# Kernel optimization log

Measured on AMD Instinct MI355X. Metric: run time of the kernel, lower is better.

## Reference

```python
import jax, jax.numpy as jnp
import numpy as np

HK, WK = 7, 11  # local_k


def _local_mask(H, W):
    # Equivalent to the torch buffer: 0 inside the hk x wk window centered on the
    # query position (for odd hk, wk), -inf outside. Shape (N, N), N = H*W.
    n = jnp.arange(H * W)
    hq, wq = n // W, n % W
    dh = jnp.abs(hq[:, None] - hq[None, :])
    dw = jnp.abs(wq[:, None] - wq[None, :])
    allowed = (dh <= HK // 2) & (dw <= WK // 2)
    return jnp.where(allowed, 0.0, -jnp.inf).astype(jnp.float32)


def setup_inputs() -> dict:
    key = jax.random.key(0)
    k1, k2, k3 = jax.random.split(key, 3)
    B, H, W, C = 8, 32, 64, 512
    N = H * W
    x = jax.random.normal(k1, (B, N, C), dtype=jnp.float32)
    qkv_w = jax.random.normal(k2, (3 * C, C), dtype=jnp.float32) * (C ** -0.5)
    proj_w = jax.random.normal(k3, (C, C), dtype=jnp.float32) * (C ** -0.5)
    proj_b = jnp.zeros((C,), dtype=jnp.float32)
    return {"x": x, "qkv_w": qkv_w, "proj_w": proj_w, "proj_b": proj_b, "H": H, "W": W}


def reference(x, qkv_w, proj_w, proj_b, H, W):
    B, N, C = x.shape
    num_heads = 8
    head_dim = C // num_heads
    scale = head_dim ** -0.5

    # qkv: Linear(dim, 3*dim, bias=False) -> (B, N, 3, heads, head_dim)
    qkv = (x @ qkv_w.T).reshape(B, N, 3, num_heads, head_dim)
    q = qkv[:, :, 0].transpose(0, 2, 1, 3) * scale  # (B, h, N, d)
    k = qkv[:, :, 1].transpose(0, 2, 1, 3)
    v = qkv[:, :, 2].transpose(0, 2, 1, 3)

    attn = jnp.einsum('bhnd,bhmd->bhnm', q, k)  # (B, h, N, N)
    attn = attn + _local_mask(H, W)  # broadcast over (B, h)
    attn = jax.nn.softmax(attn, axis=-1)

    out = jnp.einsum('bhnm,bhmd->bhnd', attn, v)  # (B, h, N, d)
    out = out.transpose(0, 2, 1, 3).reshape(B, N, C)
    return out @ proj_w.T + proj_b
```

## Files before the change

kernel.cpp:

```cpp
#include <hip/hip_runtime.h>
#include <hip/hip_bf16.h>

#define B_SZ 8
#define H_SZ 32
#define W_SZ 64
#define N_SZ 2048
#define C_SZ 512
#define NH 8
#define HD 64

using u16 = unsigned short;
typedef __attribute__((ext_vector_type(8))) short s16x8;
typedef __attribute__((ext_vector_type(4))) float f32x4;

__device__ __forceinline__ float bf2f(u16 u) {
    union { unsigned int i; float f; } c; c.i = ((unsigned int)u) << 16; return c.f;
}
__device__ __forceinline__ u16 f2bf(float f) {
    union { float f; unsigned int i; } c; c.f = f;
    unsigned int r = c.i + 0x7fffu + ((c.i >> 16) & 1u);
    return (u16)(r >> 16);
}

#define GLL16(gp, lp) __builtin_amdgcn_global_load_lds( \
    (const __attribute__((address_space(1))) unsigned int*)(gp), \
    (__attribute__((address_space(3))) unsigned int*)(lp), 16, 0, 0)

__device__ __forceinline__ int lds_off(int row, int chunk) {
    return (row * 8 + (chunk ^ (row & 7))) * 8;
}

#define NX4 2097152
#define NQ4 196608
#define NP4 65536
__global__ __launch_bounds__(256)
void conv_all(const float* __restrict__ x, const float* __restrict__ qw,
              const float* __restrict__ pw, u16* __restrict__ xb,
              u16* __restrict__ qwb, u16* __restrict__ pwb)
{
    const int i = blockIdx.x * 256 + threadIdx.x;
    const float* src; u16* dst; int idx; float sc = 1.0f;
    if (i < NX4)             { src = x;  dst = xb;  idx = i; }
    else if (i < NX4 + NQ4)  { src = qw; dst = qwb; idx = i - NX4;
                               if (idx < 65536) sc = 0.125f; }
    else                     { src = pw; dst = pwb; idx = i - NX4 - NQ4; }
    const float4 v = ((const float4*)src)[idx];
    ushort4 o = { f2bf(v.x * sc), f2bf(v.y * sc), f2bf(v.z * sc), f2bf(v.w * sc) };
    ((ushort4*)dst)[idx] = o;
}

template<int MODE, int NT>
__global__ __launch_bounds__(256)
void gemm_mfma(const u16* __restrict__ A, const u16* __restrict__ Bw,
               const float* __restrict__ bias,
               u16* __restrict__ q_ws, u16* __restrict__ k_ws, u16* __restrict__ v_ws,
               float* __restrict__ outp, int K)
{
    constexpr int NJ = (NT == 128) ? 4 : 2;
    __shared__ u16 As[128 * 64];
    __shared__ u16 Bs[NT * 64];
    const int t    = threadIdx.x;
    const int m0   = blockIdx.x * 128;
    const int n0   = blockIdx.y * NT;
    const int wave = t >> 6, lane = t & 63;
    const int wm   = (wave >> 1) << 6;
    const int wn   = (wave & 1) * (NJ * 16);
    const int l16  = lane & 15, quad = lane >> 4;
    const int srow = t >> 3;
    const int sch  = (t & 7) ^ (srow & 7);

    constexpr int AD0 = (MODE == 0) ? 4 : 2;
    f32x4 acc[AD0][4] = {};

    for (int k0 = 0; k0 < K; k0 += 64) {
        __syncthreads();
        #pragma unroll
        for (int g = 0; g < 4; ++g)
            GLL16(A + (size_t)(m0 + 32 * g + srow) * K + k0 + sch * 8,
                  &As[g * 2048 + t * 8]);
        #pragma unroll
        for (int g = 0; g < NT / 32; ++g)
            GLL16(Bw + (size_t)(n0 + 32 * g + srow) * K + k0 + sch * 8,
                  &Bs[g * 2048 + t * 8]);
        __syncthreads();

        s16x8 fx[4][2], fw[NJ][2];
        #pragma unroll
        for (int i = 0; i < 4; ++i) {
            const int R = wm + 16 * i + l16;
            fx[i][0] = *(const s16x8*)&As[lds_off(R, quad)];
            fx[i][1] = *(const s16x8*)&As[lds_off(R, 4 + quad)];
        }
        #pragma unroll
        for (int j = 0; j < NJ; ++j) {
            const int R = wn + 16 * j + l16;
            fw[j][0] = *(const s16x8*)&Bs[lds_off(R, quad)];
            fw[j][1] = *(const s16x8*)&Bs[lds_off(R, 4 + quad)];
        }
        if (MODE == 1 || n0 < 1024) {
            #pragma unroll
            for (int w = 0; w < AD0; ++w)
                #pragma unroll
                for (int x = 0; x < 4; ++x) {
                    acc[w][x] = __builtin_amdgcn_mfma_f32_16x16x32_bf16(fw[w][0], fx[x][0], acc[w][x], 0, 0, 0);
                    acc[w][x] = __builtin_amdgcn_mfma_f32_16x16x32_bf16(fw[w][1], fx[x][1], acc[w][x], 0, 0, 0);
                }
        } else {
            #pragma unroll
            for (int x = 0; x < 4; ++x)
                #pragma unroll
                for (int w = 0; w < 4; ++w) {
                    acc[x][w] = __builtin_amdgcn_mfma_f32_16x16x32_bf16(fx[x][0], fw[w][0], acc[x][w], 0, 0, 0);
                    acc[x][w] = __builtin_amdgcn_mfma_f32_16x16x32_bf16(fx[x][1], fw[w][1], acc[x][w], 0, 0, 0);
                }
        }
    }

    if (MODE == 0) {
        const int bb = m0 >> 11;
        if (n0 < 1024) {
            const int h = ((n0 + wn) >> 6) & 7;
            u16* T  = (n0 < 512) ? q_ws : k_ws;
            u16* tb = T + ((size_t)bb * NH + h) * (N_SZ * HD);
            const int nn0 = (m0 & 2047) + wm;
            const int dd0 = (quad << 2);
            #pragma unroll
            for (int w = 0; w < 4; ++w)
                #pragma unroll
                for (int x = 0; x < 4; ++x) {
                    const int nn = nn0 + 16 * x + l16;
                    ushort4 st = { f2bf(acc[w][x][0]), f2bf(acc[w][x][1]),
                                   f2bf(acc[w][x][2]), f2bf(acc[w][x][3]) };
                    *(ushort4*)(tb + (size_t)nn * HD + 16 * w + dd0) = st;
                }
        } else {
            const int nnb = (m0 & 2047) + wm + (quad << 2);
            #pragma unroll
            for (int w = 0; w < 4; ++w) {
                const int c = n0 - 1024 + wn + 16 * w + l16;
                const int h = c >> 6, dd = c & 63;
                u16* vp = v_ws + (((size_t)bb * NH + h) * HD + dd) * N_SZ + nnb;
                #pragma unroll
                for (int x = 0; x < 4; ++x) {
                    ushort4 st = { f2bf(acc[x][w][0]), f2bf(acc[x][w][1]),
                                   f2bf(acc[x][w][2]), f2bf(acc[x][w][3]) };
                    *(ushort4*)(vp + 16 * x) = st;
                }
            }
        }
    } else {
        #pragma unroll
        for (int w = 0; w < 2; ++w) {
            const int cb = n0 + wn + 16 * w + (quad << 2);
            const float4 bv = *(const float4*)&bias[cb];
            #pragma unroll
            for (int x = 0; x < 4; ++x) {
                const int gm = m0 + wm + 16 * x + l16;
                float4 st = { acc[w][x][0] + bv.x, acc[w][x][1] + bv.y,
                              acc[w][x][2] + bv.z, acc[w][x][3] + bv.w };
                *(float4*)&outp[(size_t)gm * C_SZ + cb] = st;
            }
        }
    }
}

__global__ __launch_bounds__(256)
void attn_mfma(const u16* __restrict__ q_ws, const u16* __restrict__ k_ws,
               const u16* __restrict__ vt_ws, u16* __restrict__ o_ws)
{
    __shared__ u16 KV[2][64 * 64];
    __shared__ u16 Ps[4][16 * 40];

    const int t = threadIdx.x, wave = t >> 6, lane = t & 63;
    const int l16 = lane & 15, quad = lane >> 4;
    const int u  = blockIdx.x;
    const int p  = u & 15;
    const int bh = u >> 4;
    const int r0 = 2 * p, r1 = 2 * p + 1;
    const size_t base = (size_t)bh * (N_SZ * HD);
    const int srow = t >> 3;
    const int sch  = (t & 7) ^ (srow & 7);

    const u16* qg = q_ws + base + (size_t)r0 * (64 * HD);
    u16* Qst = &KV[0][0];
    #pragma unroll
    for (int g = 0; g < 4; ++g)
        GLL16(qg + (size_t)(srow + 32 * g) * 64 + sch * 8, Qst + g * 2048 + t * 8);
    __syncthreads();

    s16x8 aQ[2][2];
    #pragma unroll
    for (int s = 0; s < 2; ++s) {
        const int Rq = 64 * s + 16 * wave + l16;
        aQ[s][0] = *(const s16x8*)&Qst[lds_off(Rq, quad)];
        aQ[s][1] = *(const s16x8*)&Qst[lds_off(Rq, 4 + quad)];
    }

    const int kb = min(max(16 * wave - 8, 0), 32);

    f32x4 accO[2][4] = {};
    float lp[2][4] = {};

    const int hlo = (r0 - 3 < 0) ? 0 : r0 - 3;
    const int hhi = (r1 + 3 > H_SZ - 1) ? H_SZ - 1 : r1 + 3;

    for (int hh = hlo; hh <= hhi; ++hh) {
        __syncthreads();
        const u16* kg = k_ws + base + (size_t)hh * (64 * HD);
        GLL16(kg + (size_t)srow        * 64 + sch * 8, &KV[0][t * 8]);
        GLL16(kg + (size_t)(srow + 32) * 64 + sch * 8, &KV[0][2048 + t * 8]);
        const u16* vg = vt_ws + base + (size_t)hh * 64;
        GLL16(vg + (size_t)srow        * N_SZ + sch * 8, &KV[1][t * 8]);
        GLL16(vg + (size_t)(srow + 32) * N_SZ + sch * 8, &KV[1][2048 + t * 8]);
        __syncthreads();

        s16x8 bK[2][2];
        #pragma unroll
        for (int j = 0; j < 2; ++j) {
            const int Rk = kb + 16 * j + l16;
            bK[j][0] = *(const s16x8*)&KV[0][lds_off(Rk, quad)];
            bK[j][1] = *(const s16x8*)&KV[0][lds_off(Rk, 4 + quad)];
        }
        s16x8 vf[4];
        #pragma unroll
        for (int j = 0; j < 4; ++j)
            vf[j] = *(const s16x8*)&KV[1][lds_off(16 * j + l16, (kb >> 3) + quad)];

        #pragma unroll
        for (int s = 0; s < 2; ++s) {
            const int dh = hh - (r0 + s);
            if (dh * dh > 9) continue;
            f32x4 z[2] = {{0.f,0.f,0.f,0.f},{0.f,0.f,0.f,0.f}};
            #pragma unroll
            for (int j = 0; j < 2; ++j) {
                z[j] = __builtin_amdgcn_mfma_f32_16x16x32_bf16(aQ[s][0], bK[j][0], z[j], 0, 0, 0);
                z[j] = __builtin_amdgcn_mfma_f32_16x16x32_bf16(aQ[s][1], bK[j][1], z[j], 0, 0, 0);
            }
            #pragma unroll
            for (int j = 0; j < 2; ++j) {
                const int ww = kb + 16 * j + l16;
                #pragma unroll
                for (int r = 0; r < 4; ++r) {
                    const int dw = ww - (16 * wave + quad * 4 + r);
                    const float pv = (dw * dw <= 25) ? __expf(z[j][r]) : 0.f;
                    const u16 pb = f2bf(pv);
                    lp[s][r] += bf2f(pb);
                    Ps[wave][(quad * 4 + r) * 40 + 16 * j + l16] = pb;
                }
            }
            s16x8 aP = *(const s16x8*)&Ps[wave][l16 * 40 + quad * 8];
            #pragma unroll
            for (int j = 0; j < 4; ++j)
                accO[s][j] = __builtin_amdgcn_mfma_f32_16x16x32_bf16(vf[j], aP, accO[s][j], 0, 0, 0);
        }
    }

    #pragma unroll
    for (int s = 0; s < 2; ++s)
        #pragma unroll
        for (int r = 0; r < 4; ++r) {
            lp[s][r] += __shfl_xor(lp[s][r], 1);
            lp[s][r] += __shfl_xor(lp[s][r], 2);
            lp[s][r] += __shfl_xor(lp[s][r], 4);
            lp[s][r] += __shfl_xor(lp[s][r], 8);
        }

    const int srcl = (l16 >> 2) << 4;
    const int rr   = l16 & 3;
    float inv[2];
    #pragma unroll
    for (int s = 0; s < 2; ++s) {
        const float a0 = __shfl(lp[s][0], srcl);
        const float a1 = __shfl(lp[s][1], srcl);
        const float a2 = __shfl(lp[s][2], srcl);
        const float a3 = __shfl(lp[s][3], srcl);
        const float lq = (rr == 0) ? a0 : (rr == 1) ? a1 : (rr == 2) ? a2 : a3;
        inv[s] = 1.0f / lq;
    }

    const int bb = bh >> 3, h = bh & 7;
    #pragma unroll
    for (int s = 0; s < 2; ++s) {
        const int row = (r0 + s) * 64 + 16 * wave + l16;
        u16* ob = o_ws + ((size_t)bb * N_SZ + row) * C_SZ + h * 64 + (quad << 2);
        #pragma unroll
        for (int j = 0; j < 4; ++j) {
            ushort4 st = { f2bf(accO[s][j][0] * inv[s]), f2bf(accO[s][j][1] * inv[s]),
                           f2bf(accO[s][j][2] * inv[s]), f2bf(accO[s][j][3] * inv[s]) };
            *(ushort4*)(ob + 16 * j) = st;
        }
    }
}

extern "C" void kernel_launch(void* const* d_in, const int* in_sizes, int n_in,
                              void* d_out, int out_size, void* d_ws, size_t ws_size,
                              hipStream_t stream)
{
    const float* x      = (const float*)d_in[0];
    const float* qkv_w  = (const float*)d_in[1];
    const float* proj_w = (const float*)d_in[2];
    const float* proj_b = (const float*)d_in[3];
    float* outp = (float*)d_out;

    const size_t seg = (size_t)B_SZ * NH * N_SZ * HD;
    u16* q_ws = (u16*)d_ws;
    u16* k_ws = q_ws + seg;
    u16* v_ws = k_ws + seg;
    u16* o_ws = v_ws + seg;
    u16* xb   = o_ws + seg;
    u16* qwb  = xb + (size_t)16384 * 512;
    u16* pwb  = qwb + (size_t)1536 * 512;

    conv_all<<<9216, 256, 0, stream>>>(x, qkv_w, proj_w, xb, qwb, pwb);

    gemm_mfma<0, 128><<<dim3(128, 12), 256, 0, stream>>>(xb, qwb, nullptr,
                                                         q_ws, k_ws, v_ws, nullptr, C_SZ);
    attn_mfma<<<B_SZ * NH * (H_SZ / 2), 256, 0, stream>>>(q_ws, k_ws, v_ws, o_ws);
    gemm_mfma<1, 64><<<dim3(128, 8), 256, 0, stream>>>(o_ws, pwb, proj_b,
                                                       nullptr, nullptr, nullptr, outp, C_SZ);
}
```

Baseline: 187.8 us.

## Split GEMM into larger-tile double-buffered QKV and projection kernels

Replaces the shared templated GEMM with two specialised kernels that use 256x256 (QKV, 512 threads) and 256x128 (projection) tiles. Each loads K in 32-wide slices through a double-buffered LDS pipeline that prefetches the next slice while computing the current one. The aim is more operand reuse per tile and hidden global-load latency. In exchange the grid is much smaller (384 and 256 blocks), which may underfill the GPU's many CUs. The V output now uses scalar 16-bit transposed stores.

```diff
diff --git a/kernel.cpp b/kernel.cpp
--- a/kernel.cpp
+++ b/kernel.cpp
@@ -21,6 +21,10 @@
     unsigned int r = c.i + 0x7fffu + ((c.i >> 16) & 1u);
     return (u16)(r >> 16);
 }
+__device__ __forceinline__ ushort4 pack4(f32x4 a) {
+    ushort4 s = { f2bf(a[0]), f2bf(a[1]), f2bf(a[2]), f2bf(a[3]) };
+    return s;
+}
 
 #define GLL16(gp, lp) __builtin_amdgcn_global_load_lds( \
     (const __attribute__((address_space(1))) unsigned int*)(gp), \
@@ -28,6 +32,9 @@
 
 __device__ __forceinline__ int lds_off(int row, int chunk) {
     return (row * 8 + (chunk ^ (row & 7))) * 8;
+}
+__device__ __forceinline__ int lds_off32(int row, int chunk) {
+    return row * 32 + (chunk ^ ((row >> 1) & 3)) * 8;
 }
 
 #define NX4 2097152
@@ -49,117 +56,145 @@
     ((ushort4*)dst)[idx] = o;
 }
 
-template<int MODE, int NT>
-__global__ __launch_bounds__(256)
-void gemm_mfma(const u16* __restrict__ A, const u16* __restrict__ Bw,
-               const float* __restrict__ bias,
-               u16* __restrict__ q_ws, u16* __restrict__ k_ws, u16* __restrict__ v_ws,
-               float* __restrict__ outp, int K)
-{
-    constexpr int NJ = (NT == 128) ? 4 : 2;
-    __shared__ u16 As[128 * 64];
-    __shared__ u16 Bs[NT * 64];
-    const int t    = threadIdx.x;
-    const int m0   = blockIdx.x * 128;
-    const int n0   = blockIdx.y * NT;
-    const int wave = t >> 6, lane = t & 63;
-    const int wm   = (wave >> 1) << 6;
-    const int wn   = (wave & 1) * (NJ * 16);
-    const int l16  = lane & 15, quad = lane >> 4;
-    const int srow = t >> 3;
-    const int sch  = (t & 7) ^ (srow & 7);
-
-    constexpr int AD0 = (MODE == 0) ? 4 : 2;
-    f32x4 acc[AD0][4] = {};
-
-    for (int k0 = 0; k0 < K; k0 += 64) {
+__global__ __launch_bounds__(512, 2)
+void gemm_qkv(const u16* __restrict__ A, const u16* __restrict__ Bw,
+              u16* __restrict__ q_ws, u16* __restrict__ k_ws, u16* __restrict__ v_ws)
+{
+    __shared__ u16 As[2][256 * 32];
+    __shared__ u16 Bs[2][256 * 32];
+    const int t = threadIdx.x;
+    const int m0 = blockIdx.x * 256;
+    const int n0 = blockIdx.y * 256;
+    const int wave = t >> 6, lane = t & 63, l16 = lane & 15, quad = lane >> 4;
+    const int wm2 = wave >> 2, wn2 = wave & 3;
+    const int srow = t >> 2;
+    const int sch  = (t & 3) ^ ((srow >> 1) & 3);
+
+    f32x4 acc[4][8] = {};
+
+    GLL16(A  + (size_t)(m0 +       srow) * C_SZ + sch * 8, &As[0][t * 8]);
+    GLL16(A  + (size_t)(m0 + 128 + srow) * C_SZ + sch * 8, &As[0][4096 + t * 8]);
+    GLL16(Bw + (size_t)(n0 +       srow) * C_SZ + sch * 8, &Bs[0][t * 8]);
+    GLL16(Bw + (size_t)(n0 + 128 + srow) * C_SZ + sch * 8, &Bs[0][4096 + t * 8]);
+
+    for (int it = 0; it < 16; ++it) {
         __syncthreads();
-        #pragma unroll
-        for (int g = 0; g < 4; ++g)
-            GLL16(A + (size_t)(m0 + 32 * g + srow) * K + k0 + sch * 8,
-                  &As[g * 2048 + t * 8]);
-        #pragma unroll
-        for (int g = 0; g < NT / 32; ++g)
-            GLL16(Bw + (size_t)(n0 + 32 * g + srow) * K + k0 + sch * 8,
-                  &Bs[g * 2048 + t * 8]);
+        if (it < 15) {
+            const int kn = (it + 1) * 32;
+            u16* an = As[(it + 1) & 1]; u16* bn = Bs[(it + 1) & 1];
+            GLL16(A  + (size_t)(m0 +       srow) * C_SZ + kn + sch * 8, an + t * 8);
+            GLL16(A  + (size_t)(m0 + 128 + srow) * C_SZ + kn + sch * 8, an + 4096 + t * 8);
+            GLL16(Bw + (size_t)(n0 +       srow) * C_SZ + kn + sch * 8, bn + t * 8);
+            GLL16(Bw + (size_t)(n0 + 128 + srow) * C_SZ + kn + sch * 8, bn + 4096 + t * 8);
+        }
+        const u16* ac = As[it & 1];
+        const u16* bc = Bs[it & 1];
+        s16x8 fw[4], fx[8];
+        #pragma unroll
+        for (int j = 0; j < 4; ++j)
+            fw[j] = *(const s16x8*)&bc[lds_off32(wn2 * 64 + 16 * j + l16, quad)];
+        #pragma unroll
+        for (int i = 0; i < 8; ++i)
+            fx[i] = *(const s16x8*)&ac[lds_off32(wm2 * 128 + 16 * i + l16, quad)];
+        #pragma unroll
+        for (int j = 0; j < 4; ++j)
+            #pragma unroll
+            for (int i = 0; i < 8; ++i)
+                acc[j][i] = __builtin_amdgcn_mfma_f32_16x16x32_bf16(fw[j], fx[i], acc[j][i], 0, 0, 0);
+    }
+
+    const int bb  = m0 >> 11;
+    const int nn0 = (m0 & 2047) + wm2 * 128;
+    if (n0 < 1024) {
+        u16* T = (n0 < 512) ? q_ws : k_ws;
+        const int h = ((n0 + wn2 * 64) >> 6) & 7;
+        u16* tb = T + ((size_t)bb * NH + h) * (N_SZ * HD);
+        #pragma unroll
+        for (int j = 0; j < 4; ++j) {
+            const int dd = 16 * j + (quad << 2);
+            #pragma unroll
+            for (int i = 0; i < 8; ++i) {
+                const int nn = nn0 + 16 * i + l16;
+                *(ushort4*)(tb + (size_t)nn * HD + dd) = pack4(acc[j][i]);
+            }
+        }
+    } else {
+        const int h = ((n0 - 1024 + wn2 * 64) >> 6) & 7;
+        u16* vb = v_ws + ((size_t)bb * NH + h) * (HD * N_SZ);
+        #pragma unroll
+        for (int j = 0; j < 4; ++j)
+            #pragma unroll
+            for (int r = 0; r < 4; ++r) {
+                const int dd = 16 * j + (quad << 2) + r;
+                u16* row = vb + (size_t)dd * N_SZ + nn0;
+                #pragma unroll
+                for (int i = 0; i < 8; ++i)
+                    row[16 * i + l16] = f2bf(acc[j][r == 0 ? i : i][r]);
+            }
+    }
+}
+
+__global__ __launch_bounds__(256, 2)
+void gemm_proj(const u16* __restrict__ A, const u16* __restrict__ Bw,
+               const float* __restrict__ bias, float* __restrict__ outp)
+{
+    __shared__ u16 As[2][256 * 32];
+    __shared__ u16 Bs[2][128 * 32];
+    const int t = threadIdx.x;
+    const int m0 = blockIdx.x * 256;
+    const int n0 = blockIdx.y * 128;
+    const int wave = t >> 6, lane = t & 63, l16 = lane & 15, quad = lane >> 4;
+    const int wm2 = wave >> 1, wn2 = wave & 1;
+    const int srow = t >> 2;
+    const int sch  = (t & 3) ^ ((srow >> 1) & 3);
+
+    f32x4 acc[4][8] = {};
+
+    #pragma unroll
+    for (int g = 0; g < 4; ++g)
+        GLL16(A + (size_t)(m0 + 64 * g + srow) * C_SZ + sch * 8, &As[0][g * 2048 + t * 8]);
+    #pragma unroll
+    for (int g = 0; g < 2; ++g)
+        GLL16(Bw + (size_t)(n0 + 64 * g + srow) * C_SZ + sch * 8, &Bs[0][g * 2048 + t * 8]);
+
+    for (int it = 0; it < 16; ++it) {
         __syncthreads();
-
-        s16x8 fx[4][2], fw[NJ][2];
-        #pragma unroll
-        for (int i = 0; i < 4; ++i) {
-            const int R = wm + 16 * i + l16;
-            fx[i][0] = *(const s16x8*)&As[lds_off(R, quad)];
-            fx[i][1] = *(const s16x8*)&As[lds_off(R, 4 + quad)];
-        }
-        #pragma unroll
-        for (int j = 0; j < NJ; ++j) {
-            const int R = wn + 16 * j + l16;
-            fw[j][0] = *(const s16x8*)&Bs[lds_off(R, quad)];
-            fw[j][1] = *(const s16x8*)&Bs[lds_off(R, 4 + quad)];
-        }
-        if (MODE == 1 || n0 < 1024) {
-            #pragma unroll
-            for (int w = 0; w < AD0; ++w)
-                #pragma unroll
-                for (int x = 0; x < 4; ++x) {
-                    acc[w][x] = __builtin_amdgcn_mfma_f32_16x16x32_bf16(fw[w][0], fx[x][0], acc[w][x], 0, 0, 0);
-                    acc[w][x] = __builtin_amdgcn_mfma_f32_16x16x32_bf16(fw[w][1], fx[x][1], acc[w][x], 0, 0, 0);
-                }
-        } else {
-            #pragma unroll
-            for (int x = 0; x < 4; ++x)
-                #pragma unroll
-                for (int w = 0; w < 4; ++w) {
-                    acc[x][w] = __builtin_amdgcn_mfma_f32_16x16x32_bf16(fx[x][0], fw[w][0], acc[x][w], 0, 0, 0);
-                    acc[x][w] = __builtin_amdgcn_mfma_f32_16x16x32_bf16(fx[x][1], fw[w][1], acc[x][w], 0, 0, 0);
-                }
-        }
-    }
-
-    if (MODE == 0) {
-        const int bb = m0 >> 11;
-        if (n0 < 1024) {
-            const int h = ((n0 + wn) >> 6) & 7;
-            u16* T  = (n0 < 512) ? q_ws : k_ws;
-            u16* tb = T + ((size_t)bb * NH + h) * (N_SZ * HD);
-            const int nn0 = (m0 & 2047) + wm;
-            const int dd0 = (quad << 2);
-            #pragma unroll
-            for (int w = 0; w < 4; ++w)
-                #pragma unroll
-                for (int x = 0; x < 4; ++x) {
-                    const int nn = nn0 + 16 * x + l16;
-                    ushort4 st = { f2bf(acc[w][x][0]), f2bf(acc[w][x][1]),
-                                   f2bf(acc[w][x][2]), f2bf(acc[w][x][3]) };
-                    *(ushort4*)(tb + (size_t)nn * HD + 16 * w + dd0) = st;
-                }
-        } else {
-            const int nnb = (m0 & 2047) + wm + (quad << 2);
-            #pragma unroll
-            for (int w = 0; w < 4; ++w) {
-                const int c = n0 - 1024 + wn + 16 * w + l16;
-                const int h = c >> 6, dd = c & 63;
-                u16* vp = v_ws + (((size_t)bb * NH + h) * HD + dd) * N_SZ + nnb;
-                #pragma unroll
-                for (int x = 0; x < 4; ++x) {
-                    ushort4 st = { f2bf(acc[x][w][0]), f2bf(acc[x][w][1]),
-                                   f2bf(acc[x][w][2]), f2bf(acc[x][w][3]) };
-                    *(ushort4*)(vp + 16 * x) = st;
-                }
-            }
-        }
-    } else {
-        #pragma unroll
-        for (int w = 0; w < 2; ++w) {
-            const int cb = n0 + wn + 16 * w + (quad << 2);
-            const float4 bv = *(const float4*)&bias[cb];
-            #pragma unroll
-            for (int x = 0; x < 4; ++x) {
-                const int gm = m0 + wm + 16 * x + l16;
-                float4 st = { acc[w][x][0] + bv.x, acc[w][x][1] + bv.y,
-                              acc[w][x][2] + bv.z, acc[w][x][3] + bv.w };
-                *(float4*)&outp[(size_t)gm * C_SZ + cb] = st;
-            }
+        if (it < 15) {
+            const int kn = (it + 1) * 32;
+            u16* an = As[(it + 1) & 1]; u16* bn = Bs[(it + 1) & 1];
+            #pragma unroll
+            for (int g = 0; g < 4; ++g)
+                GLL16(A + (size_t)(m0 + 64 * g + srow) * C_SZ + kn + sch * 8, an + g * 2048 + t * 8);
+            #pragma unroll
+            for (int g = 0; g < 2; ++g)
+                GLL16(Bw + (size_t)(n0 + 64 * g + srow) * C_SZ + kn + sch * 8, bn + g * 2048 + t * 8);
+        }
+        const u16* ac = As[it & 1];
+        const u16* bc = Bs[it & 1];
+        s16x8 fw[4], fx[8];
+        #pragma unroll
+        for (int j = 0; j < 4; ++j)
+            fw[j] = *(const s16x8*)&bc[lds_off32(wn2 * 64 + 16 * j + l16, quad)];
+        #pragma unroll
+        for (int i = 0; i < 8; ++i)
+            fx[i] = *(const s16x8*)&ac[lds_off32(wm2 * 128 + 16 * i + l16, quad)];
+        #pragma unroll
+        for (int j = 0; j < 4; ++j)
+            #pragma unroll
+            for (int i = 0; i < 8; ++i)
+                acc[j][i] = __builtin_amdgcn_mfma_f32_16x16x32_bf16(fw[j], fx[i], acc[j][i], 0, 0, 0);
+    }
+
+    #pragma unroll
+    for (int j = 0; j < 4; ++j) {
+        const int cb = n0 + wn2 * 64 + 16 * j + (quad << 2);
+        const float4 bv = *(const float4*)&bias[cb];
+        #pragma unroll
+        for (int i = 0; i < 8; ++i) {
+            const int gm = m0 + wm2 * 128 + 16 * i + l16;
+            float4 st = { acc[j][i][0] + bv.x, acc[j][i][1] + bv.y,
+                          acc[j][i][2] + bv.z, acc[j][i][3] + bv.w };
+            *(float4*)&outp[(size_t)gm * C_SZ + cb] = st;
         }
     }
 }
@@ -313,9 +348,7 @@
 
     conv_all<<<9216, 256, 0, stream>>>(x, qkv_w, proj_w, xb, qwb, pwb);
 
-    gemm_mfma<0, 128><<<dim3(128, 12), 256, 0, stream>>>(xb, qwb, nullptr,
-                                                         q_ws, k_ws, v_ws, nullptr, C_SZ);
+    gemm_qkv<<<dim3(64, 6), 512, 0, stream>>>(xb, qwb, q_ws, k_ws, v_ws);
     attn_mfma<<<B_SZ * NH * (H_SZ / 2), 256, 0, stream>>>(q_ws, k_ws, v_ws, o_ws);
-    gemm_mfma<1, 64><<<dim3(128, 8), 256, 0, stream>>>(o_ws, pwb, proj_b,
-                                                       nullptr, nullptr, nullptr, outp, C_SZ);
-}
+    gemm_proj<<<dim3(64, 4), 256, 0, stream>>>(o_ws, pwb, proj_b, outp);
+}
```

Result: slower. 198.3 us (+5.6%).
